# Kernel tuning notes

Hardware: AMD Instinct MI355X
Metric: run time of the kernel (lower is better)

Reference implementation:

```python
import jax, jax.numpy as jnp
import numpy as np

N = 100000   # nodes per side
E = 400000   # intra edges per side
EB = 400000  # bipartite (inter) edges
G = 2048     # graphs per side in the batch
FIN = 64     # input atom-feature dim
H1, C1 = 2, 64   # feature_conv: 2 heads x 64 -> 128
H2, C2 = 2, 32   # intra/inter GAT: 2 heads x 32 -> 64
D = H1 * C1      # 128


def _edges(key, e, n):
    # random edges guaranteed src != dst (PyG GATConv does remove_self_loops first)
    k1, k2 = jax.random.split(key)
    src = jax.random.randint(k1, (e,), 0, n)
    off = jax.random.randint(k2, (e,), 1, n)
    dst = (src + off) % n
    return jnp.stack([src, dst]).astype(jnp.int32)


def setup_inputs():
    key = jax.random.key(0)
    ks = iter(jax.random.split(key, 64))
    def nrm(shape, s=0.1):
        return jax.random.normal(next(ks), shape, jnp.float32) * s
    inp = {}
    inp['x_h'] = nrm((N, FIN), 1.0)
    inp['x_t'] = nrm((N, FIN), 1.0)
    inp['edge_attr_h'] = nrm((E, 64), 1.0)
    inp['edge_attr_t'] = nrm((E, 64), 1.0)
    inp['edge_index_h'] = _edges(next(ks), E, N)
    inp['edge_index_t'] = _edges(next(ks), E, N)
    inp['b_edge_index'] = _edges(next(ks), EB, N)
    inp['batch_h'] = jnp.sort(jax.random.randint(next(ks), (N,), 0, G)).astype(jnp.int32)
    inp['batch_t'] = jnp.sort(jax.random.randint(next(ks), (N,), 0, G)).astype(jnp.int32)
    inp['edge_batch_h'] = jnp.sort(jax.random.randint(next(ks), (E,), 0, G)).astype(jnp.int32)
    inp['edge_batch_t'] = jnp.sort(jax.random.randint(next(ks), (E,), 0, G)).astype(jnp.int32)
    # parameters (PyTorch Linear convention: W @ x.T, i.e. [out, in])
    inp['W_fc'] = nrm((H1 * C1, FIN)); inp['att_src_fc'] = nrm((H1, C1)); inp['att_dst_fc'] = nrm((H1, C1))
    inp['W_edge_fc'] = nrm((H1 * C1, 64)); inp['att_edge_fc'] = nrm((H1, C1)); inp['b_fc'] = jnp.zeros((H1 * C1,), jnp.float32)
    inp['W_lu'] = nrm((64, 64)); inp['b_lu'] = jnp.zeros((64,), jnp.float32)
    inp['W_intra'] = nrm((H2 * C2, D)); inp['att_src_i'] = nrm((H2, C2)); inp['att_dst_i'] = nrm((H2, C2)); inp['b_intra'] = jnp.zeros((H2 * C2,), jnp.float32)
    inp['W_int_src'] = nrm((H2 * C2, D)); inp['W_int_dst'] = nrm((H2 * C2, D)); inp['att_src_b'] = nrm((H2, C2)); inp['att_dst_b'] = nrm((H2, C2)); inp['b_inter'] = jnp.zeros((H2 * C2,), jnp.float32)
    inp['W_rel'] = nrm((1, D)); inp['b_rel'] = jnp.zeros((1,), jnp.float32); inp['W_root'] = nrm((1, D))
    inp['ln_w'] = jnp.ones((D,), jnp.float32); inp['ln_b'] = jnp.zeros((D,), jnp.float32)
    inp['W_re'] = nrm((D, 64)); inp['b_re'] = jnp.zeros((D,), jnp.float32)
    return inp


def _seg_softmax(logits, seg, n):
    m = jax.ops.segment_max(logits, seg, num_segments=n)
    m = jnp.where(jnp.isneginf(m), 0.0, m)
    e = jnp.exp(logits - m[seg])
    s = jax.ops.segment_sum(e, seg, num_segments=n)
    return e / (s[seg] + 1e-16)


def _gat(x_src, x_dst, edge_index, W_src, W_dst, a_src, a_dst, bias, H, C,
         edge_attr=None, W_edge=None, a_edge=None):
    # PyG GATConv: add_self_loops=True, negative_slope=0.2, fill_value='mean' for edge_attr
    n_dst = x_dst.shape[0]
    hs = (x_src @ W_src.T).reshape(-1, H, C)
    hd = (x_dst @ W_dst.T).reshape(-1, H, C)
    src, dst = edge_index[0], edge_index[1]
    n_loop = min(x_src.shape[0], n_dst)
    loop = jnp.arange(n_loop, dtype=src.dtype)
    src = jnp.concatenate([src, loop]); dst = jnp.concatenate([dst, loop])
    alpha = (hs * a_src).sum(-1)[src] + (hd * a_dst).sum(-1)[dst]  # [E+n, H]
    if edge_attr is not None:
        ea = jnp.concatenate([edge_attr, jnp.broadcast_to(edge_attr.mean(0), (n_loop, edge_attr.shape[1]))], 0)
        he = (ea @ W_edge.T).reshape(-1, H, C)
        alpha = alpha + (he * a_edge).sum(-1)
    alpha = jax.nn.leaky_relu(alpha, 0.2)
    alpha = _seg_softmax(alpha, dst, n_dst)
    out = jax.ops.segment_sum(hs[src] * alpha[:, :, None], dst, num_segments=n_dst)
    return out.reshape(n_dst, H * C) + bias


def _graph_ln(x, batch, w, b, n_graphs):
    # torch_geometric.nn.LayerNorm, mode='graph': normalize over all nodes+channels per graph
    F = x.shape[1]
    cnt = jax.ops.segment_sum(jnp.ones(x.shape[0], x.dtype), batch, num_segments=n_graphs)
    norm = jnp.clip(cnt, 1.0) * F
    mean = jax.ops.segment_sum(x.sum(-1), batch, num_segments=n_graphs) / norm
    xc = x - mean[batch][:, None]
    var = jax.ops.segment_sum((xc * xc).sum(-1), batch, num_segments=n_graphs) / norm
    return xc / jnp.sqrt(var + 1e-5)[batch][:, None] * w + b


def _sag_readout(x, edge_index, batch, W_rel, b_rel, W_root, n_graphs):
    # SAGPooling(min_score=-1): GraphConv score -> per-graph softmax; softmax>0>-1
    # so every node survives topk; output = global_add_pool(score-weighted x)
    src, dst = edge_index[0], edge_index[1]
    agg = jax.ops.segment_sum(x[src], dst, num_segments=x.shape[0])
    score = (agg @ W_rel.T + b_rel + x @ W_root.T)[:, 0]
    s = _seg_softmax(score, batch, n_graphs)
    return jax.ops.segment_sum(x * s[:, None], batch, num_segments=n_graphs)


def _forward(x_h, x_t, edge_attr_h, edge_attr_t, W_fc, att_src_fc, att_dst_fc, W_edge_fc, att_edge_fc, b_fc, W_lu, b_lu, W_intra, att_src_i, att_dst_i, b_intra, W_int_src, W_int_dst, att_src_b, att_dst_b, b_inter, W_rel, b_rel, W_root, ln_w, ln_b, W_re, b_re, edge_index_h, edge_index_t, b_edge_index, batch_h, batch_t, edge_batch_h, edge_batch_t):
    # shared feature GATConv with edge features
    xh = _gat(x_h, x_h, edge_index_h, W_fc, W_fc, att_src_fc, att_dst_fc, b_fc, H1, C1, edge_attr_h, W_edge_fc, att_edge_fc)
    xt = _gat(x_t, x_t, edge_index_t, W_fc, W_fc, att_src_fc, att_dst_fc, b_fc, H1, C1, edge_attr_t, W_edge_fc, att_edge_fc)
    ea_h = edge_attr_h @ W_lu.T + b_lu
    ea_t = edge_attr_t @ W_lu.T + b_lu
    # intra-graph attention: ELU then shared GATConv(128 -> 2x32)
    eh, et = jax.nn.elu(xh), jax.nn.elu(xt)
    h_intra = _gat(eh, eh, edge_index_h, W_intra, W_intra, att_src_i, att_dst_i, b_intra, H2, C2)
    t_intra = _gat(et, et, edge_index_t, W_intra, W_intra, att_src_i, att_dst_i, b_intra, H2, C2)
    # inter-graph (bipartite) attention, both directions with shared weights
    t_inter = _gat(eh, et, b_edge_index, W_int_src, W_int_dst, att_src_b, att_dst_b, b_inter, H2, C2)
    h_inter = _gat(et, eh, b_edge_index[::-1], W_int_src, W_int_dst, att_src_b, att_dst_b, b_inter, H2, C2)
    h_rep = jnp.concatenate([h_intra, h_inter], 1)  # [N, 128]
    t_rep = jnp.concatenate([t_intra, t_inter], 1)
    # SAGPooling readout + edge-graph global pooling
    h_g = _sag_readout(h_rep, edge_index_h, batch_h, W_rel, b_rel, W_root, G)
    t_g = _sag_readout(t_rep, edge_index_t, batch_t, W_rel, b_rel, W_root, G)
    h_ge = jax.nn.relu(jax.ops.segment_sum(ea_h, edge_batch_h, num_segments=G) @ W_re.T + b_re)
    t_ge = jax.nn.relu(jax.ops.segment_sum(ea_t, edge_batch_t, num_segments=G) @ W_re.T + b_re)
    h_g = h_g + h_ge
    t_g = t_g + t_ge
    h_x = jax.nn.relu(_graph_ln(h_rep, batch_h, ln_w, ln_b, G))
    t_x = jax.nn.relu(_graph_ln(t_rep, batch_t, ln_w, ln_b, G))
    return (h_x, jax.nn.relu(ea_h), t_x, jax.nn.relu(ea_t), h_g, t_g)


def reference(x_h, x_t, edge_attr_h, edge_attr_t, W_fc, att_src_fc, att_dst_fc, W_edge_fc, att_edge_fc, b_fc, W_lu, b_lu, W_intra, att_src_i, att_dst_i, b_intra, W_int_src, W_int_dst, att_src_b, att_dst_b, b_inter, W_rel, b_rel, W_root, ln_w, ln_b, W_re, b_re, edge_index_h, edge_index_t, b_edge_index, batch_h, batch_t, edge_batch_h, edge_batch_t):
    return _forward(x_h, x_t, edge_attr_h, edge_attr_t, W_fc, att_src_fc, att_dst_fc, W_edge_fc, att_edge_fc, b_fc, W_lu, b_lu, W_intra, att_src_i, att_dst_i, b_intra, W_int_src, W_int_dst, att_src_b, att_dst_b, b_inter, W_rel, b_rel, W_root, ln_w, ln_b, W_re, b_re, edge_index_h, edge_index_t, b_edge_index, batch_h, batch_t, edge_batch_h, edge_batch_t)
```

## Files before the change

kernel.cpp:

```cpp
#include <hip/hip_runtime.h>
#include <hip/hip_bf16.h>

typedef __hip_bfloat16 bf16;

#define N_  100000
#define E_  400000
#define EBI 400000
#define G_  2048
#define NP1 (N_+1)
#define SCAN_B 1024
#define SCAN_NB ((N_+SCAN_B-1)/SCAN_B)

static __device__ __forceinline__ float b2f(bf16 v){ return __bfloat162float(v); }
static __device__ __forceinline__ bf16  f2b(float v){ return __float2bfloat16(v); }
static __device__ __forceinline__ float bfu(unsigned int u){
  union{unsigned int i; float f;} x; x.i = u<<16; return x.f;
}

template<typename T> static __device__ __forceinline__ float ldv(const void* p, size_t i){
  return (float)((const T*)p)[i];
}

__global__ void k_detect(const void* x, int* flag){
  __shared__ int cnt;
// ... 63 lines not shown
__global__ void k_hist4(const int* __restrict__ ei_h,const int* __restrict__ ei_t,
                        const int* __restrict__ bei,int* cnt){
  int e = blockIdx.x*blockDim.x + threadIdx.x;
  if(e>=E_) return;
  int y = blockIdx.y;
  const int* dst = (y==0)? ei_h+E_ : (y==1)? ei_t+E_ : (y==2)? bei+EBI : bei;
  atomicAdd(&cnt[(size_t)y*N_ + dst[e]],1);
}

__global__ __launch_bounds__(256) void k_scan1(const int* __restrict__ cnt, int* rowptr, int* part){
  int g = blockIdx.y, b = blockIdx.x, t = threadIdx.x;
  const int* c = cnt + (size_t)g*N_;
  int* rp = rowptr + (size_t)g*NP1;
  int i0 = b*SCAN_B + t*4;
  int v[4];
  #pragma unroll
  for(int j=0;j<4;j++){ int i=i0+j; v[j] = (i<N_)? c[i] : 0; }
  int T = v[0]+v[1]+v[2]+v[3];
  __shared__ int sh[256];
  sh[t]=T; __syncthreads();
  int run=T;
  for(int o=1;o<256;o<<=1){
    int add = (t>=o)? sh[t-o] : 0;
    __syncthreads();
    run += add; sh[t]=run;
    __syncthreads();
  }
  int p = run - T;
  #pragma unroll
  for(int j=0;j<4;j++){ int i=i0+j; if(i<N_) rp[i]=p; p+=v[j]; }
  if(t==255) part[g*SCAN_NB + b] = run;
}

__global__ void k_scan2(int* part, int* rowptr){
  int g = blockIdx.x;
  if(threadIdx.x) return;
  int* p = part + g*SCAN_NB;
  int run=0;
  for(int i=0;i<SCAN_NB;i++){ int t=p[i]; p[i]=run; run+=t; }
  rowptr[(size_t)g*NP1 + N_] = run;
}

__global__ __launch_bounds__(256) void k_scan3(int* rowptr, const int* __restrict__ part, int* cur){
  int g=blockIdx.y, b=blockIdx.x, t=threadIdx.x;
  int base = part[g*SCAN_NB+b];
  int i0 = b*SCAN_B + t*4;
  int* rp = rowptr + (size_t)g*NP1;
  int* cu = cur + (size_t)g*N_;
  #pragma unroll
  for(int j=0;j<4;j++){ int i=i0+j; if(i<N_){ int v=rp[i]+base; rp[i]=v; cu[i]=v; } }
}

__global__ void k_fill4(const int* __restrict__ ei_h,const int* __restrict__ ei_t,
                        const int* __restrict__ bei,int* cur,int* eids,int* srcs){
  int e = blockIdx.x*blockDim.x + threadIdx.x;
  if(e>=E_) return;
  int y = blockIdx.y;
  const int *s,*d;
  if(y==0){ s=ei_h; d=ei_h+E_; }
  else if(y==1){ s=ei_t; d=ei_t+E_; }
  else if(y==2){ s=bei; d=bei+EBI; }
  else { s=bei+EBI; d=bei; }
  int dd = d[e];
  int pos = atomicAdd(&cur[(size_t)y*N_+dd],1);
  eids[(size_t)y*E_+pos]=e; srcs[(size_t)y*E_+pos]=s[e];
}

__global__ __launch_bounds__(256) void k_graph_easum(const int* dflag,
                              const void* eat_h,const void* eat_t,
                              const int* es_h,const int* ee_h,const int* es_t,const int* ee_t,
                              float* gsum_h,float* gsum_t,float* gl_h,float* gl_t){
  int g=blockIdx.x, t=threadIdx.x, side=blockIdx.y;
  const void* ea = side? eat_t : eat_h;
  int s = side? es_t[g] : es_h[g];
  int e = side? ee_t[g] : ee_h[g];
  float* gsum = side? gsum_t : gsum_h;
  float* gl   = side? gl_t : gl_h;
  int f=t&63, q=t>>6;
  float acc=0.f;
  if(*dflag){ for(int i=s+q;i<e;i+=4) acc += ((const float*)ea)[(size_t)i*64+f]; }
  else      { for(int i=s+q;i<e;i+=4) acc += b2f(((const bf16*)ea)[(size_t)i*64+f]); }
  __shared__ float red[256];
  red[t]=acc; __syncthreads();
  if(t<128) red[t]+=red[t+128];
  __syncthreads();
  if(t<64){
    float v = red[t]+red[t+64];
    gsum[(size_t)g*64+t]=v;
    atomicAdd(&gl[t], v);
  }
}

__global__ void k_loopae2(const float* sumea_h,const float* sumea_t,const float* v_edge,
                          float* lae_h,float* lae_t,float invE){
  int side=blockIdx.x; int h=threadIdx.x; if(h>=2) return;
  const float* se = side? sumea_t : sumea_h;
  float* o = side? lae_t : lae_h;
  float acc=0.f;
  for(int f=0; f<64; f++) acc += se[f]*v_edge[h*64+f];
  o[h] = acc*invE;
}

template<typename TE>
static __device__ void eags_body(int idx,const float* gsum,const int* es,const int* ee,
                                 const void* W_lu,const void* b_lu,float* ea_gs){
  int g=idx>>6, f=idx&63;
  float acc=0.f;
  for(int k=0;k<64;k++) acc += gsum[g*64+k]*ldv<TE>(W_lu,f*64+k);
  float cnt=(float)(ee[g]-es[g]);
  ea_gs[idx]=acc + cnt*ldv<TE>(b_lu,f);
}
__global__ void k_ea_gs(const int* dflag,const float* gsum_h,const float* gsum_t,
                        const int* es_h,const int* ee_h,const int* es_t,const int* ee_t,
                        const void* W_lu,const void* b_lu,float* eags_h,float* eags_t){
  int idx = blockIdx.x*blockDim.x + threadIdx.x;
  if(idx>=G_*64) return;
  int side=blockIdx.y;
  const float* gsum = side? gsum_t : gsum_h;
  const int* es = side? es_t : es_h;
  const int* ee = side? ee_t : ee_h;
  float* eags = side? eags_t : eags_h;
  if(*dflag) eags_body<float>(idx,gsum,es,ee,W_lu,b_lu,eags);
  else       eags_body<bf16 >(idx,gsum,es,ee,W_lu,b_lu,eags);
}

template<typename TE>
static __device__ void hge_body(int idx,const float* ea_gs,const void* W_re,const void* b_re,float* hge){
  int g=idx>>7, o=idx&127;
  float acc=0.f;
  for(int f=0;f<64;f++) acc += ea_gs[g*64+f]*ldv<TE>(W_re,(size_t)o*64+f);
  acc += ldv<TE>(b_re,o);
  hge[idx]=acc>0.f?acc:0.f;
}
__global__ void k_hge(const int* dflag,const float* eags_h,const float* eags_t,
                      const void* W_re,const void* b_re,float* hge_h,float* hge_t){
  int idx = blockIdx.x*blockDim.x + threadIdx.x;
  if(idx>=G_*128) return;
  int side=blockIdx.y;
  const float* eags = side? eags_t : eags_h;
  float* hge = side? hge_t : hge_h;
  if(*dflag) hge_body<float>(idx,eags,W_re,b_re,hge);
  else       hge_body<bf16 >(idx,eags,W_re,b_re,hge);
}

__global__ void k_node_alpha1(const int* dflag,const void* x_h,const void* x_t,
                              const float* __restrict__ cva,const float* __restrict__ cvb,
                              float* a1s_h,float* a1d_h,float* a1s_t,float* a1d_t){
  int i = blockIdx.x*blockDim.x + threadIdx.x;
  if(i>=N_) return;
  int side=blockIdx.y;
  const void* X = side? x_t : x_h;
  float* oa = side? a1s_t : a1s_h;
  float* ob = side? a1d_t : a1d_h;
  float a0=0,a1=0,b0=0,b1=0;
  if(*dflag){
    const float* x=(const float*)X + (size_t)i*64;
    for(int k=0;k<64;k++){ float v=x[k]; a0+=v*cva[k]; a1+=v*cva[64+k]; b0+=v*cvb[k]; b1+=v*cvb[64+k]; }
  } else {
    const bf16* x=(const bf16*)X + (size_t)i*64;
    for(int k=0;k<64;k++){ float v=b2f(x[k]); a0+=v*cva[k]; a1+=v*cva[64+k]; b0+=v*cvb[k]; b1+=v*cvb[64+k]; }
  }
  oa[i*2]=a0; oa[i*2+1]=a1; ob[i*2]=b0; ob[i*2+1]=b1;
}

__global__ void k_edge_alpha1(const int* dflag,
                              const float* a1s_h,const float* a1d_h,
                              const float* a1s_t,const float* a1d_t,
                              const int* ei_h,const int* ei_t,
                              const void* eat_h,const void* eat_t,
                              const float* __restrict__ vedge,
                              const float* lae_h,const float* lae_t,
                              float* alpha_h,float* alpha_t){
  __shared__ float sv[128];
  int t = threadIdx.x;
  if(t<128) sv[t]=vedge[t];
  __syncthreads();
  int side=blockIdx.y;
  const float* asrc = side? a1s_t : a1s_h;
  const float* adst = side? a1d_t : a1d_h;
  const int* srcI = side? ei_t : ei_h;
  const int* dstI = srcI + E_;
  const void* eattr = side? eat_t : eat_h;
  const float* loopae = side? lae_t : lae_h;
  float* alpha = side? alpha_t : alpha_h;
  int e = blockIdx.x*blockDim.x + t;
  if(e>=E_+N_) return;
  int s,d; float ae0=0.f, ae1=0.f;
  if(e<E_){
    s=srcI[e]; d=dstI[e];
    if(*dflag){
      const float4* row=(const float4*)((const float*)eattr + (size_t)e*64);
      #pragma unroll
      for(int k=0;k<16;k++){
        float4 v=row[k];
        ae0 += v.x*sv[4*k]   + v.y*sv[4*k+1]   + v.z*sv[4*k+2]   + v.w*sv[4*k+3];
        ae1 += v.x*sv[64+4*k]+ v.y*sv[64+4*k+1]+ v.z*sv[64+4*k+2]+ v.w*sv[64+4*k+3];
      }
    } else {
      const uint4* row=(const uint4*)((const bf16*)eattr + (size_t)e*64);
      #pragma unroll
      for(int k=0;k<8;k++){
        uint4 u=row[k];
        float f0=bfu(u.x&0xffffu), f1=bfu(u.x>>16), f2=bfu(u.y&0xffffu), f3=bfu(u.y>>16);
        float f4=bfu(u.z&0xffffu), f5=bfu(u.z>>16), f6=bfu(u.w&0xffffu), f7=bfu(u.w>>16);
        ae0 += f0*sv[8*k]+f1*sv[8*k+1]+f2*sv[8*k+2]+f3*sv[8*k+3]
             + f4*sv[8*k+4]+f5*sv[8*k+5]+f6*sv[8*k+6]+f7*sv[8*k+7];
        ae1 += f0*sv[64+8*k]+f1*sv[64+8*k+1]+f2*sv[64+8*k+2]+f3*sv[64+8*k+3]
             + f4*sv[64+8*k+4]+f5*sv[64+8*k+5]+f6*sv[64+8*k+6]+f7*sv[64+8*k+7];
      }
    }
  } else {
    s=d=e-E_;
    ae0=loopae[0]; ae1=loopae[1];
  }
  float l0 = asrc[s*2]  +adst[d*2]  +ae0; l0 = l0>0.f? l0 : 0.2f*l0;
  float l1 = asrc[s*2+1]+adst[d*2+1]+ae1; l1 = l1>0.f? l1 : 0.2f*l1;
  alpha[e*2]  = expf(fminf(l0,50.f));
  alpha[e*2+1]= expf(fminf(l1,50.f));
}

__global__ void k_edge_alpha2(const float* ais_h,const float* aid_h,
                              const float* ais_t,const float* aid_t,
                              const float* abs_h,const float* abd_h,
                              const float* abs_t,const float* abd_t,
                              const int* ei_h,const int* ei_t,const int* bei,
                              float* a_ih,float* a_it,float* a_bt,float* a_bh){
  int e = blockIdx.x*blockDim.x + threadIdx.x;
  if(e>=E_+N_) return;
  int y = blockIdx.y;
  const float *asrc,*adst; const int *srcI,*dstI; float* alpha;
  if(y==0){ asrc=ais_h; adst=aid_h; srcI=ei_h;    dstI=ei_h+E_;  alpha=a_ih; }
  else if(y==1){ asrc=ais_t; adst=aid_t; srcI=ei_t; dstI=ei_t+E_; alpha=a_it; }
  else if(y==2){ asrc=abs_h; adst=abd_t; srcI=bei;  dstI=bei+EBI; alpha=a_bt; }
  else { asrc=abs_t; adst=abd_h; srcI=bei+EBI; dstI=bei; alpha=a_bh; }
  int s,d;
  if(e<E_){ s=srcI[e]; d=dstI[e]; } else { s=d=e-E_; }
  float l0 = asrc[s*2]  +adst[d*2];   l0 = l0>0.f? l0 : 0.2f*l0;
  float l1 = asrc[s*2+1]+adst[d*2+1]; l1 = l1>0.f? l1 : 0.2f*l1;
  alpha[e*2]  = expf(fminf(l0,50.f));
  alpha[e*2+1]= expf(fminf(l1,50.f));
}

__global__ __launch_bounds__(256) void k_gatherA(const int* dflag,
    const void* x_h,const void* x_t,
    const float* alpha_h,const float* alpha_t,
    const int* rp0,const int* eid0,const int* src0,
    const int* rp1,const int* eid1,const int* src1,
    float* C,float* D){
  int t=threadIdx.x, side=blockIdx.y;
  int d=blockIdx.x*2 + (t>>7);
  if(d>=N_) return;
  const void* X = side? x_t : x_h;
  const float* alpha = side? alpha_t : alpha_h;
  const int* rp  = side? rp1  : rp0;
  const int* eid = side? eid1 : eid0;
  const int* src = side? src1 : src0;
  float* out = side? D : C;
  int ch=t&127, h=ch>>6, f=ch&63;
  int f32=*dflag;
  int j0=rp[d], j1=rp[d+1];
  float acc=0.f, ss=0.f;
  for(int j=j0;j<j1;j++){
    int e=eid[j], s=src[j];
    float a=alpha[(size_t)e*2+h];
    float xv = f32? ((const float*)X)[(size_t)s*64+f] : b2f(((const bf16*)X)[(size_t)s*64+f]);
    acc+=xv*a; ss+=a;
  }
  {
    float a=alpha[((size_t)E_+d)*2+h];
    float xv = f32? ((const float*)X)[(size_t)d*64+f] : b2f(((const bf16*)X)[(size_t)d*64+f]);
    acc+=xv*a; ss+=a;
  }
  out[(size_t)d*128+ch]=acc/(ss+1e-16f);
}

__global__ __launch_bounds__(256) void k_headelu(const int* dflag,
    const float* __restrict__ C,const float* __restrict__ D,
    const void* W, const void* bias, bf16* eh, bf16* et){
  __shared__ float sA[64*68];
  __shared__ float sW[64*68];
  __shared__ float sB[64];
  const int t = threadIdx.x;
  const int half = blockIdx.y;
  const int side = blockIdx.z;
  const int n0 = blockIdx.x*64;
  const int f32 = *dflag;
  const float* acc = side? D : C;
  bf16* out = side? et : eh;
  for(int i=t;i<4096;i+=256){
    int o=i>>6, k=i&63;
    float v = f32 ? ((const float*)W)[(size_t)(half*64+o)*64+k]
                  : b2f(((const bf16*)W)[(size_t)(half*64+o)*64+k]);
    int om = (o>>2) | ((o&3)<<4);
    sW[om*68+k] = v;
  }
  if(t<64) sB[t] = f32 ? ((const float*)bias)[half*64+t] : b2f(((const bf16*)bias)[half*64+t]);
  for(int i=t;i<1024;i+=256){
    int m=i>>4, k4=i&15;
    int n=n0+m;
    float4 v = make_float4(0.f,0.f,0.f,0.f);
    if(n<N_) v = *(const float4*)&acc[((size_t)(2*n+half))*64 + k4*4];
    *(float4*)&sA[m*68 + k4*4] = v;
  }
  __syncthreads();
  const int cg = t&15, rg = t>>4;
  float s[4][4];
  #pragma unroll
  for(int i=0;i<4;i++)
    #pragma unroll
    for(int j=0;j<4;j++) s[i][j]=0.f;
  #pragma unroll 4
  for(int k0=0;k0<64;k0+=4){
    float4 a[4], w[4];
    #pragma unroll
    for(int i=0;i<4;i++) a[i] = *(const float4*)&sA[(rg+16*i)*68 + k0];
    #pragma unroll
    for(int j=0;j<4;j++) w[j] = *(const float4*)&sW[(cg+16*j)*68 + k0];
    #pragma unroll
    for(int i=0;i<4;i++)
      #pragma unroll
      for(int j=0;j<4;j++)
        s[i][j] += a[i].x*w[j].x + a[i].y*w[j].y + a[i].z*w[j].z + a[i].w*w[j].w;
  }
  #pragma unroll
  for(int i=0;i<4;i++){
    int n = n0 + rg + 16*i;
// ... 62 lines not shown
    for(int k=0;k<128;k++) acc += sA[row*132+k]*scv[v*132+k];
    if(n<N_){
      float* o = (v<2)? ais : (v<4)? aid : (v<6)? ab_s : ab_d;
      o[(size_t)n*2+(v&1)]=acc;
    }
  }
  const int cg=t&15, rg=t>>4;
  for(int chunk=0;chunk<2;chunk++){
    const void* W = chunk? W_bs : W_i;
    bf16* out = chunk? msgB : msgI;
    float s[4][4];
    #pragma unroll
    for(int i=0;i<4;i++)
      #pragma unroll
      for(int j=0;j<4;j++) s[i][j]=0.f;
    for(int kc=0;kc<128;kc+=64){
      __syncthreads();
      for(int i=t;i<4096;i+=256){
        int o=i>>6,k=i&63;
        float v = f32? ((const float*)W)[(size_t)o*128+kc+k] : b2f(((const bf16*)W)[(size_t)o*128+kc+k]);
        int om=(o>>2)|((o&3)<<4);
        sW[om*68+k]=v;
      }
      __syncthreads();
      #pragma unroll 4
      for(int k0=0;k0<64;k0+=4){
        float4 a[4], w[4];
        #pragma unroll
        for(int i=0;i<4;i++) a[i] = *(const float4*)&sA[(rg+16*i)*132 + kc + k0];
        #pragma unroll
        for(int j=0;j<4;j++) w[j] = *(const float4*)&sW[(cg+16*j)*68 + k0];
        #pragma unroll
        for(int i=0;i<4;i++)
          #pragma unroll
          for(int j=0;j<4;j++)
            s[i][j] += a[i].x*w[j].x + a[i].y*w[j].y + a[i].z*w[j].z + a[i].w*w[j].w;
      }
    }
    #pragma unroll
    for(int i=0;i<4;i++){
      int n = n0 + rg + 16*i;
      if(n>=N_) continue;
      union { bf16 h[4]; uint2 u; } pk;
      #pragma unroll
      for(int j=0;j<4;j++) pk.h[j]=f2b(s[i][j]);
      *(uint2*)&out[(size_t)n*64 + 4*cg] = pk.u;
    }
  }
}

__global__ __launch_bounds__(256) void k_gather_rep(const int* dflag,
    const bf16* msgI_h,const bf16* msgI_t,const bf16* msgB_h,const bf16* msgB_t,
    const float* a_ih,const float* a_it,const float* a_bt,const float* a_bh,
    const int* rp0,const int* eid0,const int* src0,
    const int* rp1,const int* eid1,const int* src1,
    const int* rp2,const int* eid2,const int* src2,
    const int* rp3,const int* eid3,const int* src3,
    const void* b_intra,const void* b_inter,
    const void* W_rel,const void* b_rel,const void* W_root,
    float* h_rep,float* t_rep,
    float* z_h,float* z_t,float* sc_h,float* sc_t){
  int t=threadIdx.x, side=blockIdx.y;
  int d=blockIdx.x*2 + (t>>7);
  int ch=t&127, half=ch>>6, ch64=ch&63, hh=ch64>>5;
  const bf16* msg; const float* alpha; const int *rp,*eid,*src; const void* bias;
  float *rep,*z,*sc;
  if(side==0){
    rep=h_rep; z=z_h; sc=sc_h;
    if(half==0){ msg=msgI_h; alpha=a_ih; rp=rp0; eid=eid0; src=src0; bias=b_intra; }
    else       { msg=msgB_t; alpha=a_bh; rp=rp3; eid=eid3; src=src3; bias=b_inter; }
  } else {
    rep=t_rep; z=z_t; sc=sc_t;
    if(half==0){ msg=msgI_t; alpha=a_it; rp=rp1; eid=eid1; src=src1; bias=b_intra; }
    else       { msg=msgB_h; alpha=a_bt; rp=rp2; eid=eid2; src=src2; bias=b_inter; }
  }
  int f32=*dflag;
  float repv=0.f;
  if(d<N_){
    int j0=rp[d], j1=rp[d+1];
    float acc=0.f, ss=0.f;
    for(int j=j0;j<j1;j++){
      int e=eid[j], s=src[j];
      float a=alpha[(size_t)e*2+hh];
      acc += b2f(msg[(size_t)s*64+ch64])*a; ss+=a;
    }
    float a=alpha[((size_t)E_+d)*2+hh];
    acc += b2f(msg[(size_t)d*64+ch64])*a; ss+=a;
    float b = f32? ((const float*)bias)[ch64] : b2f(((const bf16*)bias)[ch64]);
    repv = acc/(ss+1e-16f)+b;
    rep[(size_t)d*128+ch]=repv;
  }
  float wrel = f32? ((const float*)W_rel)[ch] : b2f(((const bf16*)W_rel)[ch]);
  float wroot= f32? ((const float*)W_root)[ch]: b2f(((const bf16*)W_root)[ch]);
  __shared__ float sz[256], sr[256];
  sz[t]=repv*wrel; sr[t]=repv*wroot;
  __syncthreads();
  for(int w=64;w>0;w>>=1){
    if((t&127)<w){ sz[t]+=sz[t+w]; sr[t]+=sr[t+w]; }
    __syncthreads();
  }
  if((t&127)==0 && d<N_){
    float br = f32? ((const float*)b_rel)[0] : b2f(((const bf16*)b_rel)[0]);
    z[d]=sz[t];
    sc[d]=sr[t]+br;
  }
}

__global__ void k_score_gather(const float* z_h,const float* z_t,
    const int* rp0,const int* src0,const int* rp1,const int* src1,
    float* sc_h,float* sc_t){
  int i = blockIdx.x*blockDim.x + threadIdx.x;
  if(i>=N_) return;
  int side=blockIdx.y;
  const float* z = side? z_t : z_h;
  const int* rp = side? rp1 : rp0;
  const int* sr = side? src1 : src0;
  float* sc = side? sc_t : sc_h;
  float a=0.f;
  for(int j=rp[i];j<rp[i+1];j++) a += z[sr[j]];
  sc[i]+=a;
}

__global__ __launch_bounds__(128) void k_finalize(const int* dflag,
    const float* __restrict__ h_rep,const float* __restrict__ t_rep,
    const float* __restrict__ sc_h,const float* __restrict__ sc_t,
    const int* ns_h,const int* ne_h,const int* ns_t,const int* ne_t,
    const float* __restrict__ hge_h,const float* __restrict__ hge_t,
    const void* lnw,const void* lnb,
    void* out,size_t o_hg,size_t o_tg,size_t o_hx,size_t o_tx){
  int g=blockIdx.x, side=blockIdx.y, tid=threadIdx.x;
  const float* rep = side? t_rep : h_rep;
  const float* sc  = side? sc_t  : sc_h;
  const float* hge = side? hge_t : hge_h;
  int s = side? ns_t[g] : ns_h[g];
  int e = side? ne_t[g] : ne_h[g];
  size_t og = side? o_tg : o_hg;
  size_t ox = side? o_tx : o_hx;
  __shared__ float red[128];
  float m=-1e30f;
  for(int n=s+tid;n<e;n+=128) m=fmaxf(m,sc[n]);
  red[tid]=m; __syncthreads();
  for(int w=64;w>0;w>>=1){ if(tid<w) red[tid]=fmaxf(red[tid],red[tid+w]); __syncthreads(); }
  float M=red[0]; __syncthreads();
  float den=0.f;
  for(int n=s+tid;n<e;n+=128) den += expf(sc[n]-M);
  red[tid]=den; __syncthreads();
  for(int w=64;w>0;w>>=1){ if(tid<w) red[tid]+=red[tid+w]; __syncthreads(); }
  den=red[0]; __syncthreads();
  float sm=0.f,sq=0.f;
  for(int n=s;n<e;n++){ float v=rep[(size_t)n*128+tid]; sm+=v; sq+=v*v; }
  red[tid]=sm; __syncthreads();
  for(int w=64;w>0;w>>=1){ if(tid<w) red[tid]+=red[tid+w]; __syncthreads(); }
  float S=red[0]; __syncthreads();
  red[tid]=sq; __syncthreads();
  for(int w=64;w>0;w>>=1){ if(tid<w) red[tid]+=red[tid+w]; __syncthreads(); }
  float SQ=red[0];
  float cntf=(float)(e-s);
// ... 106 lines not shown
  const int*  ei_h     = (const int*)d_in[4];
  const int*  ei_t     = (const int*)d_in[5];
  const int*  bei      = (const int*)d_in[6];
  const int*  batch_h  = (const int*)d_in[7];
  const int*  batch_t  = (const int*)d_in[8];
  const int*  ebat_h   = (const int*)d_in[9];
  const int*  ebat_t   = (const int*)d_in[10];
  const void* W_fc     = d_in[11];
  const void* a_s_fc   = d_in[12];
  const void* a_d_fc   = d_in[13];
  const void* W_e      = d_in[14];
  const void* a_e      = d_in[15];
  const void* b_fc     = d_in[16];
  const void* W_lu     = d_in[17];
  const void* b_lu     = d_in[18];
  const void* W_i      = d_in[19];
  const void* a_s_i    = d_in[20];
  const void* a_d_i    = d_in[21];
  const void* b_intra  = d_in[22];
  const void* W_bs     = d_in[23];
  const void* W_bd     = d_in[24];
  const void* a_s_b    = d_in[25];
  const void* a_d_b    = d_in[26];
  const void* b_inter  = d_in[27];
  const void* W_rel    = d_in[28];
  const void* b_rel    = d_in[29];
  const void* W_root   = d_in[30];
  const void* ln_w     = d_in[31];
  const void* ln_b     = d_in[32];
  const void* W_re     = d_in[33];
  const void* b_re     = d_in[34];

  const size_t o_hx  = 0;
  const size_t o_eah = (size_t)N_*128;
  const size_t o_tx  = o_eah + (size_t)E_*64;
  const size_t o_eat = o_tx  + (size_t)N_*128;
  const size_t o_hg  = o_eat + (size_t)E_*64;
  const size_t o_tg  = o_hg  + (size_t)G_*128;

  bf16* eh   = (bf16*)d_out + o_hx;
  bf16* et   = (bf16*)d_out + o_tx;
  bf16* msgI_h = (bf16*)d_out + o_eah;
  bf16* msgI_t = msgI_h + (size_t)N_*64;
  bf16* msgB_h = msgI_h + (size_t)2*N_*64;
  bf16* msgB_t = msgI_h + (size_t)3*N_*64;
  float* areg  = (float*)((bf16*)d_out + o_eat);
  float* alpha1_h  = areg;
  float* alpha1_t  = areg + (size_t)(E_+N_)*2;
  float* alpha2_ih = areg + (size_t)2*(E_+N_)*2;
  float* alpha2_it = areg + (size_t)3*(E_+N_)*2;
  float* alpha2_bt = alpha1_h;
  float* alpha2_bh = alpha1_t;
  int* csr_base = (int*)(areg + (size_t)4*(E_+N_)*2);
  int* eids = csr_base;
  int* srcs = csr_base + (size_t)4*E_;
  int* eid0 = eids;                 int* eid1 = eids + (size_t)E_;
  int* eid2 = eids + (size_t)2*E_;  int* eid3 = eids + (size_t)3*E_;
  int* src0 = srcs;                 int* src1 = srcs + (size_t)E_;
  int* src2 = srcs + (size_t)2*E_;  int* src3 = srcs + (size_t)3*E_;

  char* p = (char*)d_ws;
  size_t off = 0;
  auto alloc = [&](size_t bytes)->char*{
    char* r = p + off; off += (bytes + 255) & ~(size_t)255; return r;
  };
  int* dflag=(int*)alloc(256);
  int* es_h = (int*)alloc(G_*4); int* ee_h = (int*)alloc(G_*4);
  int* es_t = (int*)alloc(G_*4); int* ee_t = (int*)alloc(G_*4);
  int* ns_h = (int*)alloc(G_*4); int* ne_h = (int*)alloc(G_*4);
  int* ns_t = (int*)alloc(G_*4); int* ne_t = (int*)alloc(G_*4);
  float* sumea_h = (float*)alloc(64*4);
  float* sumea_t = (float*)alloc(64*4);
  float* c_fc_s=(float*)alloc(128*4); float* c_fc_d=(float*)alloc(128*4);
  float* v_edge=(float*)alloc(128*4);
  float* c_i_s=(float*)alloc(256*4);  float* c_i_d=(float*)alloc(256*4);
  float* c_b_s=(float*)alloc(256*4);  float* c_b_d=(float*)alloc(256*4);
  float* lae_h=(float*)alloc(2*4);    float* lae_t=(float*)alloc(2*4);
  int* cnt    = (int*)alloc((size_t)4*N_*4);
  int* cur    = (int*)alloc((size_t)4*N_*4);
  int* rowptr = (int*)alloc((size_t)4*NP1*4);
  int* part   = (int*)alloc((size_t)4*SCAN_NB*4);
  float* a1s_h=(float*)alloc((size_t)N_*2*4); float* a1d_h=(float*)alloc((size_t)N_*2*4);
  float* a1s_t=(float*)alloc((size_t)N_*2*4); float* a1d_t=(float*)alloc((size_t)N_*2*4);
  float* ais_h=(float*)alloc((size_t)N_*2*4); float* aid_h=(float*)alloc((size_t)N_*2*4);
  float* ais_t=(float*)alloc((size_t)N_*2*4); float* aid_t=(float*)alloc((size_t)N_*2*4);
  float* abs_h=(float*)alloc((size_t)N_*2*4); float* abd_h=(float*)alloc((size_t)N_*2*4);
  float* abs_t=(float*)alloc((size_t)N_*2*4); float* abd_t=(float*)alloc((size_t)N_*2*4);
  float* z_h=(float*)alloc((size_t)N_*4); float* z_t=(float*)alloc((size_t)N_*4);
  float* sc_h=(float*)alloc((size_t)N_*4); float* sc_t=(float*)alloc((size_t)N_*4);
  float* gsum_h=(float*)alloc((size_t)G_*64*4); float* gsum_t=(float*)alloc((size_t)G_*64*4);
  float* eags_h=(float*)alloc((size_t)G_*64*4); float* eags_t=(float*)alloc((size_t)G_*64*4);
  float* hge_h =(float*)alloc((size_t)G_*128*4); float* hge_t =(float*)alloc((size_t)G_*128*4);
  float* C = (float*)alloc((size_t)N_*128*4);
  float* D = (float*)alloc((size_t)N_*128*4);
  float* t_rep = C;
  float* h_rep = D;

  int* rp0 = rowptr;                  int* rp1 = rowptr + (size_t)NP1;
  int* rp2 = rowptr + (size_t)2*NP1;  int* rp3 = rowptr + (size_t)3*NP1;

  auto cdiv=[](long a, long b){ return (int)((a+b-1)/b); };

  k_detect<<<1,256,0,stream>>>(x_h, dflag);
  hipMemsetAsync(es_h, 0, (size_t)G_*4*8, stream);
  hipMemsetAsync(sumea_h, 0, 512, stream);
  hipMemsetAsync(cnt, 0, (size_t)4*N_*4, stream);

  k_combine<<<6,256,0,stream>>>(dflag, W_fc,a_s_fc,a_d_fc, W_e,a_e, W_i,a_s_i,a_d_i,
                                W_bs,W_bd,a_s_b,a_d_b,
                                c_fc_s,c_fc_d,v_edge,c_i_s,c_i_d,c_b_s,c_b_d);
  k_ranges4<<<dim3(cdiv(E_,256),4),256,0,stream>>>(ebat_h,ebat_t,batch_h,batch_t,
                                es_h,ee_h,es_t,ee_t,ns_h,ne_h,ns_t,ne_t);

  k_hist4<<<dim3(cdiv(E_,256),4),256,0,stream>>>(ei_h, ei_t, bei, cnt);
  k_scan1<<<dim3(SCAN_NB,4),256,0,stream>>>(cnt, rowptr, part);
  k_scan2<<<4,32,0,stream>>>(part, rowptr);
  k_scan3<<<dim3(SCAN_NB,4),256,0,stream>>>(rowptr, part, cur);
  k_fill4<<<dim3(cdiv(E_,256),4),256,0,stream>>>(ei_h, ei_t, bei, cur, eids, srcs);

  k_graph_easum<<<dim3(G_,2),256,0,stream>>>(dflag, eat_h,eat_t, es_h,ee_h,es_t,ee_t,
                                gsum_h,gsum_t, sumea_h,sumea_t);
  k_loopae2<<<2,64,0,stream>>>(sumea_h, sumea_t, v_edge, lae_h, lae_t, 1.f/(float)E_);
  k_ea_gs<<<dim3(cdiv(G_*64,256),2),256,0,stream>>>(dflag, gsum_h,gsum_t,
                                es_h,ee_h,es_t,ee_t, W_lu, b_lu, eags_h, eags_t);
  k_hge<<<dim3(cdiv(G_*128,256),2),256,0,stream>>>(dflag, eags_h, eags_t, W_re, b_re, hge_h, hge_t);

  k_node_alpha1<<<dim3(cdiv(N_,256),2),256,0,stream>>>(dflag, x_h, x_t, c_fc_s, c_fc_d,
                                a1s_h, a1d_h, a1s_t, a1d_t);
  k_edge_alpha1<<<dim3(cdiv(E_+N_,256),2),256,0,stream>>>(dflag, a1s_h,a1d_h,a1s_t,a1d_t,
                                ei_h, ei_t, eat_h, eat_t, v_edge, lae_h, lae_t,
                                alpha1_h, alpha1_t);
  k_gatherA<<<dim3(cdiv(N_,2),2),256,0,stream>>>(dflag, x_h, x_t, alpha1_h, alpha1_t,
                                rp0, eid0, src0, rp1, eid1, src1, C, D);
  k_headelu<<<dim3(cdiv(N_,64),2,2),256,0,stream>>>(dflag, C, D, W_fc, b_fc, eh, et);

  k_msg_alpha<<<dim3(cdiv(N_,64),2),256,0,stream>>>(dflag, eh, et, W_i, W_bs,
                                c_i_s, c_i_d, c_b_s, c_b_d,
                                msgI_h, msgI_t, msgB_h, msgB_t,
                                ais_h, aid_h, abs_h, abd_h,
                                ais_t, aid_t, abs_t, abd_t);
  k_edge_alpha2<<<dim3(cdiv(E_+N_,256),4),256,0,stream>>>(ais_h,aid_h,ais_t,aid_t,
                                abs_h,abd_h,abs_t,abd_t, ei_h, ei_t, bei,
                                alpha2_ih, alpha2_it, alpha2_bt, alpha2_bh);

  k_gather_rep<<<dim3(cdiv(N_,2),2),256,0,stream>>>(dflag,
                                msgI_h, msgI_t, msgB_h, msgB_t,
                                alpha2_ih, alpha2_it, alpha2_bt, alpha2_bh,
                                rp0, eid0, src0, rp1, eid1, src1,
                                rp2, eid2, src2, rp3, eid3, src3,
                                b_intra, b_inter, W_rel, b_rel, W_root,
                                h_rep, t_rep, z_h, z_t, sc_h, sc_t);
  k_score_gather<<<dim3(cdiv(N_,256),2),256,0,stream>>>(z_h, z_t, rp0, src0, rp1, src1, sc_h, sc_t);

  k_finalize<<<dim3(G_,2),128,0,stream>>>(dflag, h_rep, t_rep, sc_h, sc_t,
                                ns_h, ne_h, ns_t, ne_t, hge_h, hge_t,
                                ln_w, ln_b, d_out, o_hg, o_tg, o_hx, o_tx);

  k_ea_final<<<dim3(E_/64,2),256,0,stream>>>(dflag, eat_h, eat_t, W_lu, b_lu,
                                d_out, o_eah, o_eat);

  (void)in_sizes; (void)n_in; (void)out_size; (void)ws_size;
}
```

Measured before the change: 1.975 ms.

## Store edge alphas in CSR order and vectorize per-destination gather kernels

k_fill4 now records each edge's CSR position instead of an edge-id array. The alpha kernels scatter their results directly into CSR order, so the gather kernels read alpha contiguously and no longer need the eid indirection. k_gatherA and k_gather_rep are restructured so each thread handles 4 channels with vector loads, two edges per iteration, and more destination nodes per block. k_gather_rep replaces its shared-memory reduction with wave shuffles. The cost moves into scattered alpha writes in the alpha kernels.

```diff
diff --git a/kernel.cpp b/kernel.cpp
--- a/kernel.cpp
+++ b/kernel.cpp
@@ -139,7 +139,7 @@
 }
 
 __global__ void k_fill4(const int* __restrict__ ei_h,const int* __restrict__ ei_t,
-                        const int* __restrict__ bei,int* cur,int* eids,int* srcs){
+                        const int* __restrict__ bei,int* cur,int* poss,int* srcs){
   int e = blockIdx.x*blockDim.x + threadIdx.x;
   if(e>=E_) return;
   int y = blockIdx.y;
@@ -150,7 +150,8 @@
   else { s=bei+EBI; d=bei; }
   int dd = d[e];
   int pos = atomicAdd(&cur[(size_t)y*N_+dd],1);
-  eids[(size_t)y*E_+pos]=e; srcs[(size_t)y*E_+pos]=s[e];
+  srcs[(size_t)y*E_+pos]=s[e];
+  poss[(size_t)y*E_+e]=pos;
 }
 
 __global__ __launch_bounds__(256) void k_graph_easum(const int* dflag,
@@ -257,6 +258,7 @@
                               const void* eat_h,const void* eat_t,
                               const float* __restrict__ vedge,
                               const float* lae_h,const float* lae_t,
+                              const int* pos0,const int* pos1,
                               float* alpha_h,float* alpha_t){
   __shared__ float sv[128];
   int t = threadIdx.x;
@@ -269,6 +271,7 @@
   const int* dstI = srcI + E_;
   const void* eattr = side? eat_t : eat_h;
   const float* loopae = side? lae_t : lae_h;
+  const int* pos = side? pos1 : pos0;
   float* alpha = side? alpha_t : alpha_h;
   int e = blockIdx.x*blockDim.x + t;
   if(e>=E_+N_) return;
@@ -302,8 +305,10 @@
   }
   float l0 = asrc[s*2]  +adst[d*2]  +ae0; l0 = l0>0.f? l0 : 0.2f*l0;
   float l1 = asrc[s*2+1]+adst[d*2+1]+ae1; l1 = l1>0.f? l1 : 0.2f*l1;
-  alpha[e*2]  = expf(fminf(l0,50.f));
-  alpha[e*2+1]= expf(fminf(l1,50.f));
+  float e0 = expf(fminf(l0,50.f));
+  float e1 = expf(fminf(l1,50.f));
+  size_t w = (e<E_)? (size_t)pos[e] : (size_t)e;
+  *(float2*)&alpha[w*2] = make_float2(e0,e1);
 }
 
 __global__ void k_edge_alpha2(const float* ais_h,const float* aid_h,
@@ -311,6 +316,7 @@
                               const float* abs_h,const float* abd_h,
                               const float* abs_t,const float* abd_t,
                               const int* ei_h,const int* ei_t,const int* bei,
+                              const int* poss,
                               float* a_ih,float* a_it,float* a_bt,float* a_bh){
   int e = blockIdx.x*blockDim.x + threadIdx.x;
   if(e>=E_+N_) return;
@@ -320,45 +326,94 @@
   else if(y==1){ asrc=ais_t; adst=aid_t; srcI=ei_t; dstI=ei_t+E_; alpha=a_it; }
   else if(y==2){ asrc=abs_h; adst=abd_t; srcI=bei;  dstI=bei+EBI; alpha=a_bt; }
   else { asrc=abs_t; adst=abd_h; srcI=bei+EBI; dstI=bei; alpha=a_bh; }
+  const int* pos = poss + (size_t)y*E_;
   int s,d;
   if(e<E_){ s=srcI[e]; d=dstI[e]; } else { s=d=e-E_; }
   float l0 = asrc[s*2]  +adst[d*2];   l0 = l0>0.f? l0 : 0.2f*l0;
   float l1 = asrc[s*2+1]+adst[d*2+1]; l1 = l1>0.f? l1 : 0.2f*l1;
-  alpha[e*2]  = expf(fminf(l0,50.f));
-  alpha[e*2+1]= expf(fminf(l1,50.f));
+  float e0 = expf(fminf(l0,50.f));
+  float e1 = expf(fminf(l1,50.f));
+  size_t w = (e<E_)? (size_t)pos[e] : (size_t)e;
+  *(float2*)&alpha[w*2] = make_float2(e0,e1);
 }
 
 __global__ __launch_bounds__(256) void k_gatherA(const int* dflag,
     const void* x_h,const void* x_t,
     const float* alpha_h,const float* alpha_t,
-    const int* rp0,const int* eid0,const int* src0,
-    const int* rp1,const int* eid1,const int* src1,
+    const int* rp0,const int* src0,
+    const int* rp1,const int* src1,
     float* C,float* D){
   int t=threadIdx.x, side=blockIdx.y;
-  int d=blockIdx.x*2 + (t>>7);
+  int d=blockIdx.x*16 + (t>>4);
   if(d>=N_) return;
+  int f4=(t&15)*4;
   const void* X = side? x_t : x_h;
   const float* alpha = side? alpha_t : alpha_h;
   const int* rp  = side? rp1  : rp0;
-  const int* eid = side? eid1 : eid0;
   const int* src = side? src1 : src0;
   float* out = side? D : C;
-  int ch=t&127, h=ch>>6, f=ch&63;
   int f32=*dflag;
   int j0=rp[d], j1=rp[d+1];
-  float acc=0.f, ss=0.f;
-  for(int j=j0;j<j1;j++){
-    int e=eid[j], s=src[j];
-    float a=alpha[(size_t)e*2+h];
-    float xv = f32? ((const float*)X)[(size_t)s*64+f] : b2f(((const bf16*)X)[(size_t)s*64+f]);
-    acc+=xv*a; ss+=a;
+  float acc0[4]={0,0,0,0}, acc1[4]={0,0,0,0};
+  float ss0=0.f, ss1=0.f;
+  int j=j0;
+  for(; j+1<j1; j+=2){
+    int s0=src[j], s1=src[j+1];
+    float2 a0=*(const float2*)&alpha[(size_t)j*2];
+    float2 a1=*(const float2*)&alpha[(size_t)(j+1)*2];
+    float x0[4], x1[4];
+    if(f32){
+      float4 v0=*(const float4*)((const float*)X+(size_t)s0*64+f4);
+      float4 v1=*(const float4*)((const float*)X+(size_t)s1*64+f4);
+      x0[0]=v0.x; x0[1]=v0.y; x0[2]=v0.z; x0[3]=v0.w;
+      x1[0]=v1.x; x1[1]=v1.y; x1[2]=v1.z; x1[3]=v1.w;
+    } else {
+      uint2 u0=*(const uint2*)((const bf16*)X+(size_t)s0*64+f4);
+      uint2 u1=*(const uint2*)((const bf16*)X+(size_t)s1*64+f4);
+      x0[0]=bfu(u0.x&0xffffu); x0[1]=bfu(u0.x>>16); x0[2]=bfu(u0.y&0xffffu); x0[3]=bfu(u0.y>>16);
+      x1[0]=bfu(u1.x&0xffffu); x1[1]=bfu(u1.x>>16); x1[2]=bfu(u1.y&0xffffu); x1[3]=bfu(u1.y>>16);
+    }
+    #pragma unroll
+    for(int c=0;c<4;c++){
+      acc0[c] += x0[c]*a0.x + x1[c]*a1.x;
+      acc1[c] += x0[c]*a0.y + x1[c]*a1.y;
+    }
+    ss0+=a0.x+a1.x; ss1+=a0.y+a1.y;
+  }
+  if(j<j1){
+    int s0=src[j];
+    float2 a0=*(const float2*)&alpha[(size_t)j*2];
+    float x0[4];
+    if(f32){
+      float4 v0=*(const float4*)((const float*)X+(size_t)s0*64+f4);
+      x0[0]=v0.x; x0[1]=v0.y; x0[2]=v0.z; x0[3]=v0.w;
+    } else {
+      uint2 u0=*(const uint2*)((const bf16*)X+(size_t)s0*64+f4);
+      x0[0]=bfu(u0.x&0xffffu); x0[1]=bfu(u0.x>>16); x0[2]=bfu(u0.y&0xffffu); x0[3]=bfu(u0.y>>16);
+    }
+    #pragma unroll
+    for(int c=0;c<4;c++){ acc0[c]+=x0[c]*a0.x; acc1[c]+=x0[c]*a0.y; }
+    ss0+=a0.x; ss1+=a0.y;
   }
   {
-    float a=alpha[((size_t)E_+d)*2+h];
-    float xv = f32? ((const float*)X)[(size_t)d*64+f] : b2f(((const bf16*)X)[(size_t)d*64+f]);
-    acc+=xv*a; ss+=a;
-  }
-  out[(size_t)d*128+ch]=acc/(ss+1e-16f);
+    float2 a=*(const float2*)&alpha[((size_t)E_+d)*2];
+    float xv[4];
+    if(f32){
+      float4 v=*(const float4*)((const float*)X+(size_t)d*64+f4);
+      xv[0]=v.x; xv[1]=v.y; xv[2]=v.z; xv[3]=v.w;
+    } else {
+      uint2 u=*(const uint2*)((const bf16*)X+(size_t)d*64+f4);
+      xv[0]=bfu(u.x&0xffffu); xv[1]=bfu(u.x>>16); xv[2]=bfu(u.y&0xffffu); xv[3]=bfu(u.y>>16);
+    }
+    #pragma unroll
+    for(int c=0;c<4;c++){ acc0[c]+=xv[c]*a.x; acc1[c]+=xv[c]*a.y; }
+    ss0+=a.x; ss1+=a.y;
+  }
+  float i0=1.f/(ss0+1e-16f), i1=1.f/(ss1+1e-16f);
+  float4 o0 = make_float4(acc0[0]*i0,acc0[1]*i0,acc0[2]*i0,acc0[3]*i0);
+  float4 o1 = make_float4(acc1[0]*i1,acc1[1]*i1,acc1[2]*i1,acc1[3]*i1);
+  *(float4*)&out[(size_t)d*128+f4]    = o0;
+  *(float4*)&out[(size_t)d*128+64+f4] = o1;
 }
 
 __global__ __launch_bounds__(256) void k_headelu(const int* dflag,
@@ -527,57 +582,86 @@
 __global__ __launch_bounds__(256) void k_gather_rep(const int* dflag,
     const bf16* msgI_h,const bf16* msgI_t,const bf16* msgB_h,const bf16* msgB_t,
     const float* a_ih,const float* a_it,const float* a_bt,const float* a_bh,
-    const int* rp0,const int* eid0,const int* src0,
-    const int* rp1,const int* eid1,const int* src1,
-    const int* rp2,const int* eid2,const int* src2,
-    const int* rp3,const int* eid3,const int* src3,
+    const int* rp0,const int* src0,
+    const int* rp1,const int* src1,
+    const int* rp2,const int* src2,
+    const int* rp3,const int* src3,
     const void* b_intra,const void* b_inter,
     const void* W_rel,const void* b_rel,const void* W_root,
     float* h_rep,float* t_rep,
     float* z_h,float* z_t,float* sc_h,float* sc_t){
   int t=threadIdx.x, side=blockIdx.y;
-  int d=blockIdx.x*2 + (t>>7);
-  int ch=t&127, half=ch>>6, ch64=ch&63, hh=ch64>>5;
-  const bf16* msg; const float* alpha; const int *rp,*eid,*src; const void* bias;
+  int d=blockIdx.x*8 + (t>>5);
+  if(d>=N_) return;
+  int g=t&31, half=g>>4, l=g&15, ch64=l*4, hh=l>>3;
+  const bf16* msg; const float* alpha; const int *rp,*src; const void* bias;
   float *rep,*z,*sc;
   if(side==0){
     rep=h_rep; z=z_h; sc=sc_h;
-    if(half==0){ msg=msgI_h; alpha=a_ih; rp=rp0; eid=eid0; src=src0; bias=b_intra; }
-    else       { msg=msgB_t; alpha=a_bh; rp=rp3; eid=eid3; src=src3; bias=b_inter; }
+    if(half==0){ msg=msgI_h; alpha=a_ih; rp=rp0; src=src0; bias=b_intra; }
+    else       { msg=msgB_t; alpha=a_bh; rp=rp3; src=src3; bias=b_inter; }
   } else {
     rep=t_rep; z=z_t; sc=sc_t;
-    if(half==0){ msg=msgI_t; alpha=a_it; rp=rp1; eid=eid1; src=src1; bias=b_intra; }
-    else       { msg=msgB_h; alpha=a_bt; rp=rp2; eid=eid2; src=src2; bias=b_inter; }
+    if(half==0){ msg=msgI_t; alpha=a_it; rp=rp1; src=src1; bias=b_intra; }
+    else       { msg=msgB_h; alpha=a_bt; rp=rp2; src=src2; bias=b_inter; }
   }
   int f32=*dflag;
-  float repv=0.f;
-  if(d<N_){
-    int j0=rp[d], j1=rp[d+1];
-    float acc=0.f, ss=0.f;
-    for(int j=j0;j<j1;j++){
-      int e=eid[j], s=src[j];
-      float a=alpha[(size_t)e*2+hh];
-      acc += b2f(msg[(size_t)s*64+ch64])*a; ss+=a;
-    }
+  int j0=rp[d], j1=rp[d+1];
+  float acc[4]={0,0,0,0};
+  float ss=0.f;
+  int j=j0;
+  for(; j+1<j1; j+=2){
+    int s0=src[j], s1=src[j+1];
+    float a0=alpha[(size_t)j*2+hh];
+    float a1=alpha[(size_t)(j+1)*2+hh];
+    uint2 m0=*(const uint2*)&msg[(size_t)s0*64+ch64];
+    uint2 m1=*(const uint2*)&msg[(size_t)s1*64+ch64];
+    acc[0]+=bfu(m0.x&0xffffu)*a0 + bfu(m1.x&0xffffu)*a1;
+    acc[1]+=bfu(m0.x>>16)*a0     + bfu(m1.x>>16)*a1;
+    acc[2]+=bfu(m0.y&0xffffu)*a0 + bfu(m1.y&0xffffu)*a1;
+    acc[3]+=bfu(m0.y>>16)*a0     + bfu(m1.y>>16)*a1;
+    ss+=a0+a1;
+  }
+  if(j<j1){
+    int s0=src[j];
+    float a0=alpha[(size_t)j*2+hh];
+    uint2 m0=*(const uint2*)&msg[(size_t)s0*64+ch64];
+    acc[0]+=bfu(m0.x&0xffffu)*a0;
+    acc[1]+=bfu(m0.x>>16)*a0;
+    acc[2]+=bfu(m0.y&0xffffu)*a0;
+    acc[3]+=bfu(m0.y>>16)*a0;
+    ss+=a0;
+  }
+  {
     float a=alpha[((size_t)E_+d)*2+hh];
-    acc += b2f(msg[(size_t)d*64+ch64])*a; ss+=a;
-    float b = f32? ((const float*)bias)[ch64] : b2f(((const bf16*)bias)[ch64]);
-    repv = acc/(ss+1e-16f)+b;
-    rep[(size_t)d*128+ch]=repv;
-  }
-  float wrel = f32? ((const float*)W_rel)[ch] : b2f(((const bf16*)W_rel)[ch]);
-  float wroot= f32? ((const float*)W_root)[ch]: b2f(((const bf16*)W_root)[ch]);
-  __shared__ float sz[256], sr[256];
-  sz[t]=repv*wrel; sr[t]=repv*wroot;
-  __syncthreads();
-  for(int w=64;w>0;w>>=1){
-    if((t&127)<w){ sz[t]+=sz[t+w]; sr[t]+=sr[t+w]; }
-    __syncthreads();
-  }
-  if((t&127)==0 && d<N_){
+    uint2 m=*(const uint2*)&msg[(size_t)d*64+ch64];
+    acc[0]+=bfu(m.x&0xffffu)*a;
+    acc[1]+=bfu(m.x>>16)*a;
+    acc[2]+=bfu(m.y&0xffffu)*a;
+    acc[3]+=bfu(m.y>>16)*a;
+    ss+=a;
+  }
+  float inv=1.f/(ss+1e-16f);
+  float repv[4];
+  #pragma unroll
+  for(int c=0;c<4;c++){
+    float b = f32? ((const float*)bias)[ch64+c] : b2f(((const bf16*)bias)[ch64+c]);
+    repv[c]=acc[c]*inv+b;
+  }
+  *(float4*)&rep[(size_t)d*128 + half*64 + ch64] = make_float4(repv[0],repv[1],repv[2],repv[3]);
+  float pz=0.f, pr=0.f;
+  #pragma unroll
+  for(int c=0;c<4;c++){
+    int ch = half*64+ch64+c;
+    float wrel = f32? ((const float*)W_rel)[ch] : b2f(((const bf16*)W_rel)[ch]);
+    float wroot= f32? ((const float*)W_root)[ch]: b2f(((const bf16*)W_root)[ch]);
+    pz += repv[c]*wrel; pr += repv[c]*wroot;
+  }
+  #pragma unroll
+  for(int m=1;m<=16;m<<=1){ pz+=__shfl_xor(pz,m); pr+=__shfl_xor(pr,m); }
+  if(g==0){
     float br = f32? ((const float*)b_rel)[0] : b2f(((const bf16*)b_rel)[0]);
-    z[d]=sz[t];
-    sc[d]=sr[t]+br;
+    z[d]=pz; sc[d]=pr+br;
   }
 }
 
@@ -790,10 +874,9 @@
   float* alpha2_bt = alpha1_h;
   float* alpha2_bh = alpha1_t;
   int* csr_base = (int*)(areg + (size_t)4*(E_+N_)*2);
-  int* eids = csr_base;
+  int* poss = csr_base;
   int* srcs = csr_base + (size_t)4*E_;
-  int* eid0 = eids;                 int* eid1 = eids + (size_t)E_;
-  int* eid2 = eids + (size_t)2*E_;  int* eid3 = eids + (size_t)3*E_;
+  int* pos0 = poss;                 int* pos1 = poss + (size_t)E_;
   int* src0 = srcs;                 int* src1 = srcs + (size_t)E_;
   int* src2 = srcs + (size_t)2*E_;  int* src3 = srcs + (size_t)3*E_;
 
@@ -854,7 +937,7 @@
   k_scan1<<<dim3(SCAN_NB,4),256,0,stream>>>(cnt, rowptr, part);
   k_scan2<<<4,32,0,stream>>>(part, rowptr);
   k_scan3<<<dim3(SCAN_NB,4),256,0,stream>>>(rowptr, part, cur);
-  k_fill4<<<dim3(cdiv(E_,256),4),256,0,stream>>>(ei_h, ei_t, bei, cur, eids, srcs);
+  k_fill4<<<dim3(cdiv(E_,256),4),256,0,stream>>>(ei_h, ei_t, bei, cur, poss, srcs);
 
   k_graph_easum<<<dim3(G_,2),256,0,stream>>>(dflag, eat_h,eat_t, es_h,ee_h,es_t,ee_t,
                                 gsum_h,gsum_t, sumea_h,sumea_t);
@@ -867,9 +950,9 @@
                                 a1s_h, a1d_h, a1s_t, a1d_t);
   k_edge_alpha1<<<dim3(cdiv(E_+N_,256),2),256,0,stream>>>(dflag, a1s_h,a1d_h,a1s_t,a1d_t,
                                 ei_h, ei_t, eat_h, eat_t, v_edge, lae_h, lae_t,
-                                alpha1_h, alpha1_t);
-  k_gatherA<<<dim3(cdiv(N_,2),2),256,0,stream>>>(dflag, x_h, x_t, alpha1_h, alpha1_t,
-                                rp0, eid0, src0, rp1, eid1, src1, C, D);
+                                pos0, pos1, alpha1_h, alpha1_t);
+  k_gatherA<<<dim3(cdiv(N_,16),2),256,0,stream>>>(dflag, x_h, x_t, alpha1_h, alpha1_t,
+                                rp0, src0, rp1, src1, C, D);
   k_headelu<<<dim3(cdiv(N_,64),2,2),256,0,stream>>>(dflag, C, D, W_fc, b_fc, eh, et);
 
   k_msg_alpha<<<dim3(cdiv(N_,64),2),256,0,stream>>>(dflag, eh, et, W_i, W_bs,
@@ -878,14 +961,13 @@
                                 ais_h, aid_h, abs_h, abd_h,
                                 ais_t, aid_t, abs_t, abd_t);
   k_edge_alpha2<<<dim3(cdiv(E_+N_,256),4),256,0,stream>>>(ais_h,aid_h,ais_t,aid_t,
-                                abs_h,abd_h,abs_t,abd_t, ei_h, ei_t, bei,
+                                abs_h,abd_h,abs_t,abd_t, ei_h, ei_t, bei, poss,
                                 alpha2_ih, alpha2_it, alpha2_bt, alpha2_bh);
 
-  k_gather_rep<<<dim3(cdiv(N_,2),2),256,0,stream>>>(dflag,
+  k_gather_rep<<<dim3(cdiv(N_,8),2),256,0,stream>>>(dflag,
                                 msgI_h, msgI_t, msgB_h, msgB_t,
                                 alpha2_ih, alpha2_it, alpha2_bt, alpha2_bh,
-                                rp0, eid0, src0, rp1, eid1, src1,
-                                rp2, eid2, src2, rp3, eid3, src3,
+                                rp0, src0, rp1, src1, rp2, src2, rp3, src3,
                                 b_intra, b_inter, W_rel, b_rel, W_root,
                                 h_rep, t_rep, z_h, z_t, sc_h, sc_t);
   k_score_gather<<<dim3(cdiv(N_,256),2),256,0,stream>>>(z_h, z_t, rp0, src0, rp1, src1, sc_h, sc_t);
```

After: 1.605 ms. 18.8% less time.
